# Optimization experiments

Hardware: AMD Instinct MI355X
Metric: run time of the kernel (lower is better)

The kernel has to match this reference:

```python
import jax, jax.numpy as jnp
import numpy as np

N, E = 50000, 800000
F_NODE, F_EDGE, H, LAT, MAXN = 128, 16, 128, 64, 200


def setup_inputs() -> dict:
    key = jax.random.key(0)
    ks = jax.random.split(key, 40)
    s = 0.05
    p = {
        'x': jax.random.normal(ks[0], (N, F_NODE), jnp.float32),
        'edge_index': jax.random.randint(ks[1], (2, E), 0, N, jnp.int64),
        'edge_attr': jax.random.normal(ks[2], (E, F_EDGE), jnp.float32),
        'eps': jax.random.normal(ks[3], (1, LAT), jnp.float32),
        'num_nodes': N,
        # GATConv layer 1 (heads=1)
        'W1': jax.random.normal(ks[4], (F_NODE, H), jnp.float32) * s,
        'att_src1': jax.random.normal(ks[5], (H,), jnp.float32) * s,
        'att_dst1': jax.random.normal(ks[6], (H,), jnp.float32) * s,
        'We1': jax.random.normal(ks[7], (F_EDGE, H), jnp.float32) * s,
        'att_e1': jax.random.normal(ks[8], (H,), jnp.float32) * s,
        'b1': jnp.zeros((H,), jnp.float32),
        # GATConv layer 2
        'W2': jax.random.normal(ks[9], (H, H), jnp.float32) * s,
        'att_src2': jax.random.normal(ks[10], (H,), jnp.float32) * s,
        'att_dst2': jax.random.normal(ks[11], (H,), jnp.float32) * s,
        'We2': jax.random.normal(ks[12], (F_EDGE, H), jnp.float32) * s,
        'att_e2': jax.random.normal(ks[13], (H,), jnp.float32) * s,
        'b2': jnp.zeros((H,), jnp.float32),
        # heads
        'mu_W': jax.random.normal(ks[14], (H, LAT), jnp.float32) * s,
        'mu_b': jnp.zeros((LAT,), jnp.float32),
        'lv_W': jax.random.normal(ks[15], (H, LAT), jnp.float32) * s,
        'lv_b': jnp.zeros((LAT,), jnp.float32),
        'dec_W': jax.random.normal(ks[16], (LAT, H), jnp.float32) * s,
        'dec_b': jnp.zeros((H,), jnp.float32),
        'adj_W1': jax.random.normal(ks[17], (H, H), jnp.float32) * s,
        'adj_b1': jnp.zeros((H,), jnp.float32),
        'adj_W2': jax.random.normal(ks[18], (H, MAXN), jnp.float32) * s,
        'adj_b2': jnp.zeros((MAXN,), jnp.float32),
        'nd_W1': jax.random.normal(ks[19], (H, H), jnp.float32) * s,
        'nd_b1': jnp.zeros((H,), jnp.float32),
        'nd_W2': jax.random.normal(ks[20], (H, F_NODE), jnp.float32) * s,
        'nd_b2': jnp.zeros((F_NODE,), jnp.float32),
    }
    return p


def _gat(h, src, dst, ea, W, a_s, a_d, We, a_e, b, n):
    # PyG GATConv, heads=1: linear transform, per-edge attention, segment softmax over dst
    g = h @ W                                     # [n, H]
    alpha = jax.nn.leaky_relu((g @ a_s)[src] + (g @ a_d)[dst] + (ea @ We) @ a_e,
                              negative_slope=0.2)  # [E']
    m = jax.ops.segment_max(alpha, dst, num_segments=n)
    ex = jnp.exp(alpha - m[dst])
    den = jax.ops.segment_sum(ex, dst, num_segments=n)
    w = ex / den[dst]
    return jax.ops.segment_sum(w[:, None] * g[src], dst, num_segments=n) + b


def _forward(x, edge_index, edge_attr, eps, num_nodes,
             W1, att_src1, att_dst1, We1, att_e1, b1,
             W2, att_src2, att_dst2, We2, att_e2, b2,
             mu_W, mu_b, lv_W, lv_b, dec_W, dec_b,
             adj_W1, adj_b1, adj_W2, adj_b2, nd_W1, nd_b1, nd_W2, nd_b2):
    n = x.shape[0]
    src, dst = edge_index[0], edge_index[1]
    # add self loops; self-loop edge_attr = per-node mean of incoming edge_attr (PyG fill_value='mean')
    deg = jax.ops.segment_sum(jnp.ones((src.shape[0],), x.dtype), dst, num_segments=n)
    mean_ea = jax.ops.segment_sum(edge_attr, dst, num_segments=n) / jnp.maximum(deg, 1.0)[:, None]
    loop = jnp.arange(n)
    src_f = jnp.concatenate([src, loop])
    dst_f = jnp.concatenate([dst, loop])
    ea_f = jnp.concatenate([edge_attr, mean_ea])
    h = jax.nn.relu(_gat(x, src_f, dst_f, ea_f, W1, att_src1, att_dst1, We1, att_e1, b1, n))
    h = jax.nn.relu(_gat(h, src_f, dst_f, ea_f, W2, att_src2, att_dst2, We2, att_e2, b2, n))
    hg = h.mean(axis=0, keepdims=True)            # global_mean_pool, single graph -> [1, H]
    mu = hg @ mu_W + mu_b
    logvar = hg @ lv_W + lv_b
    z = mu + eps * jnp.exp(0.5 * logvar)
    hd = jax.nn.relu(z @ dec_W + dec_b)           # [1, H]
    hn = jnp.broadcast_to(hd[:, None, :], (1, num_nodes, hd.shape[-1]))
    adj = jax.nn.relu(hn @ adj_W1 + adj_b1) @ adj_W2 + adj_b2   # [1, n, MAXN]
    adj = adj[:, :, :num_nodes]
    nodes = jax.nn.relu(hn @ nd_W1 + nd_b1) @ nd_W2 + nd_b2     # [1, n, F_NODE]
    return adj, nodes, mu, logvar


def reference(x, edge_index, edge_attr, eps, num_nodes,
              W1, att_src1, att_dst1, We1, att_e1, b1,
              W2, att_src2, att_dst2, We2, att_e2, b2,
              mu_W, mu_b, lv_W, lv_b, dec_W, dec_b,
              adj_W1, adj_b1, adj_W2, adj_b2, nd_W1, nd_b1, nd_W2, nd_b2):
    return _forward(x, edge_index, edge_attr, eps, num_nodes,
                    W1, att_src1, att_dst1, We1, att_e1, b1,
                    W2, att_src2, att_dst2, We2, att_e2, b2,
                    mu_W, mu_b, lv_W, lv_b, dec_W, dec_b,
                    adj_W1, adj_b1, adj_W2, adj_b2, nd_W1, nd_b1, nd_W2, nd_b2)
```

## Files before the change

kernel.cpp:

```cpp
#include <hip/hip_runtime.h>
#include <math.h>

#define NN   50000
#define EE   800000
#define EF   850000
#define HH   128
#define FE   16
#define LATD 64
#define MAXNN 200

#define ADJ_TOT   10000000
#define NODES_TOT 6400000
#define OUT_TOT   16400000
#define MU_OFF    16400000
#define LV_OFF    16400064

#define GEMMBLOCKS 782
#define DEGBLOCKS  782
#define NBSCAN     49

typedef __attribute__((ext_vector_type(8))) short bf16x8;
typedef __attribute__((ext_vector_type(4))) float f32x4;
typedef __attribute__((ext_vector_type(2))) float f32x2;

__device__ __forceinline__ unsigned short f2bf(float f){
  unsigned int u = __float_as_uint(f);
  unsigned int r = (u + 0x7FFFu + ((u>>16)&1u)) >> 16;
  return (unsigned short)r;
}
__device__ __forceinline__ float bf2f(unsigned short h){
  return __uint_as_float(((unsigned int)h)<<16);
}

__global__ __launch_bounds__(256) void kprep(int* ideg, float* hgsum,
                       const float* We1, const float* ae1, const float* We2, const float* ae2,
                       float* wa1, float* wa2,
                       const float* W1, const float* W2,
                       unsigned short* Wp1, unsigned short* Wp2){
  int i = blockIdx.x*256 + threadIdx.x;
  if(i < NN) ideg[i]=0;
  if(i < HH) hgsum[i]=0.f;
  if(i < FE){
    float s1=0.f, s2=0.f;
    for(int j=0;j<HH;j++){ s1 += We1[i*HH+j]*ae1[j]; s2 += We2[i*HH+j]*ae2[j]; }
    wa1[i]=s1; wa2[i]=s2;
  }
  if(i < HH*HH){
    int n = i >> 7, k = i & 127;
    Wp1[i] = f2bf(W1[k*HH + n]);
    Wp2[i] = f2bf(W2[k*HH + n]);
  }
}

__device__ __forceinline__ void gemm_body(int bid, int tid, const void* __restrict__ hin, int h_is_fp32,
    const unsigned short* __restrict__ Wp,
    const float* __restrict__ atts, const float* __restrict__ attd,
    unsigned char* __restrict__ A8, float* __restrict__ asrc, float* __restrict__ adst){
  int lane = tid & 63;
  int wid  = tid >> 6;
  int l = lane & 15, q = lane >> 4;
  int r0 = bid*64 + wid*16;
  if(r0 >= NN) return;
  const unsigned short* hb = (const unsigned short*)hin;
  const float*          hf = (const float*)hin;
  int row = r0 + l;

  bf16x8 afr[4];
  if(h_is_fp32){
    float4 u[8];
    #pragma unroll
    for(int kb=0;kb<4;kb++){
      const float* p = hf + (size_t)row*HH + kb*32 + q*8;
      u[kb*2]   = *(const float4*)(p);
      u[kb*2+1] = *(const float4*)(p+4);
    }
    #pragma unroll
    for(int kb=0;kb<4;kb++){
      afr[kb][0]=(short)f2bf(u[kb*2].x);   afr[kb][1]=(short)f2bf(u[kb*2].y);
      afr[kb][2]=(short)f2bf(u[kb*2].z);   afr[kb][3]=(short)f2bf(u[kb*2].w);
      afr[kb][4]=(short)f2bf(u[kb*2+1].x); afr[kb][5]=(short)f2bf(u[kb*2+1].y);
      afr[kb][6]=(short)f2bf(u[kb*2+1].z); afr[kb][7]=(short)f2bf(u[kb*2+1].w);
    }
  } else {
    #pragma unroll
    for(int kb=0;kb<4;kb++)
      afr[kb] = *(const bf16x8*)(hb + (size_t)row*HH + kb*32 + q*8);
  }

  f32x4 acc[8];
  #pragma unroll
  for(int t=0;t<8;t++) acc[t]=(f32x4){0.f,0.f,0.f,0.f};

  #pragma unroll
  for(int kb=0;kb<4;kb++){
    #pragma unroll
    for(int t=0;t<8;t++){
      bf16x8 b = *(const bf16x8*)(Wp + (size_t)(t*16+l)*HH + kb*32 + q*8);
      acc[t] = __builtin_amdgcn_mfma_f32_16x16x32_bf16(afr[kb], b, acc[t], 0,0,0);
    }
  }

  float av[8], dv[8];
  #pragma unroll
  for(int t=0;t<8;t++){ av[t]=atts[t*16+l]; dv[t]=attd[t*16+l]; }
  #pragma unroll
  for(int reg=0;reg<4;reg++){
    float ps=0.f, pd=0.f;
    #pragma unroll
    for(int t=0;t<8;t++){ ps+=acc[t][reg]*av[t]; pd+=acc[t][reg]*dv[t]; }
    #pragma unroll
    for(int m=8;m>=1;m>>=1){ ps+=__shfl_xor(ps,m,16); pd+=__shfl_xor(pd,m,16); }
    if(l==0){ int R=r0+q*4+reg; asrc[R]=ps; adst[R]=pd; }
  }
  #pragma unroll
  for(int t=0;t<8;t++)
    #pragma unroll
    for(int reg=0;reg<4;reg++){
      int pk = __builtin_amdgcn_cvt_pk_fp8_f32(acc[t][reg], 0.f, 0, false);
      A8[(size_t)(r0+q*4+reg)*HH + t*16 + l] = (unsigned char)(pk & 0xFF);
    }
}

__global__ __launch_bounds__(256) void kgemm3(const void* __restrict__ hin, int h_is_fp32,
    const unsigned short* __restrict__ Wp,
    const float* __restrict__ atts, const float* __restrict__ attd,
    unsigned char* __restrict__ A8, float* __restrict__ asrc, float* __restrict__ adst){
  gemm_body(blockIdx.x, threadIdx.x, hin, h_is_fp32, Wp, atts, attd, A8, asrc, adst);
}

__global__ __launch_bounds__(256) void kdeggemm(
    const int* __restrict__ ei, int* ideg, unsigned short* __restrict__ erank,
    const void* __restrict__ hin, int h_is_fp32,
    const unsigned short* __restrict__ Wp,
    const float* __restrict__ atts, const float* __restrict__ attd,
    unsigned char* __restrict__ A8, float* __restrict__ asrc, float* __restrict__ adst){
  if(blockIdx.x < GEMMBLOCKS){
    gemm_body(blockIdx.x, threadIdx.x, hin, h_is_fp32, Wp, atts, attd, A8, asrc, adst);
  } else {
    int e0 = ((blockIdx.x - GEMMBLOCKS)*256 + threadIdx.x)*4;
    if(e0 + 3 < EE){
      int4 d4 = *(const int4*)(ei + EE + e0);
      unsigned short r0 = (unsigned short)atomicAdd(&ideg[d4.x], 1);
      unsigned short r1 = (unsigned short)atomicAdd(&ideg[d4.y], 1);
      unsigned short r2 = (unsigned short)atomicAdd(&ideg[d4.z], 1);
      unsigned short r3 = (unsigned short)atomicAdd(&ideg[d4.w], 1);
      ushort4 rr; rr.x=r0; rr.y=r1; rr.z=r2; rr.w=r3;
      *(ushort4*)(erank + e0) = rr;
    } else {
      for(int j=0;j<4;j++)
        if(e0+j < EE) erank[e0+j] = (unsigned short)atomicAdd(&ideg[ei[EE+e0+j]], 1);
    }
  }
}

__global__ void kscan1(const int* __restrict__ ideg, int* rowstart, int* blocksum){
  __shared__ int sd[1024];
  int t=threadIdx.x; int i=blockIdx.x*1024+t;
  int v = (i<NN)? (ideg[i]+1) : 0;
  sd[t]=v; __syncthreads();
  for(int off=1; off<1024; off<<=1){
    int x = (t>=off)? sd[t-off] : 0;
    __syncthreads();
    sd[t] += x;
    __syncthreads();
  }
  if(i<NN) rowstart[i] = sd[t]-v;
  if(t==1023) blocksum[blockIdx.x]=sd[1023];
}
__global__ __launch_bounds__(256) void kscan3i(int* rowstart, const int* __restrict__ blocksum){
  __shared__ int bo[64];
  int t = threadIdx.x;
  if(t < 64){
    int v = (t < NBSCAN)? blocksum[t] : 0;
    int inc = v;
    #pragma unroll
    for(int off=1; off<64; off<<=1){
      int x = __shfl_up(inc, off);
      if(t>=off) inc += x;
    }
    bo[t] = inc - v;
  }
  __syncthreads();
  int i = blockIdx.x*256 + t;
  if(i<NN) rowstart[i] += bo[i>>10];
  if(i==0) rowstart[NN] = bo[NBSCAN];
}

__device__ __forceinline__ unsigned etpack(const float4* a4,
                         const float* __restrict__ wa1, const float* __restrict__ wa2){
  float4 v0=a4[0], v1=a4[1], v2=a4[2], v3=a4[3];
  float va[16]={v0.x,v0.y,v0.z,v0.w, v1.x,v1.y,v1.z,v1.w,
                v2.x,v2.y,v2.z,v2.w, v3.x,v3.y,v3.z,v3.w};
  float d1=0.f,d2=0.f;
  #pragma unroll
  for(int f=0;f<FE;f++){ d1+=va[f]*wa1[f]; d2+=va[f]*wa2[f]; }
  return (unsigned)f2bf(d1) | ((unsigned)f2bf(d2)<<16);
}
__global__ __launch_bounds__(256) void kscatter(const int* __restrict__ ei, const float* __restrict__ ea,
                         const float* __restrict__ wa1, const float* __restrict__ wa2,
                         const int* __restrict__ rowstart, const unsigned short* __restrict__ erank,
                         uint2* __restrict__ csr){
  int e0 = (blockIdx.x*256 + threadIdx.x)*2;
  if(e0>=EE) return;
  int sA=ei[e0],    sB=ei[e0+1];
  int dA=ei[EE+e0], dB=ei[EE+e0+1];
  int rA=(int)erank[e0], rB=(int)erank[e0+1];
  int pA=rowstart[dA]+rA, pB=rowstart[dB]+rB;
  const float4* a4 = (const float4*)(ea + (size_t)e0*FE);
  unsigned yA = etpack(a4,   wa1, wa2);
  unsigned yB = etpack(a4+4, wa1, wa2);
  uint2 enA; enA.x=(unsigned)sA; enA.y=yA;
  uint2 enB; enB.x=(unsigned)sB; enB.y=yB;
  csr[pA]=enA; csr[pB]=enB;
}

__global__ __launch_bounds__(256) void kgat(const unsigned char* __restrict__ A8,
    const float* __restrict__ asrc, const float* __restrict__ adst,
    const int* __restrict__ rowstart, uint2* __restrict__ csr,
    int mode, const float* __restrict__ bias,
    float* __restrict__ alphabuf, int* __restrict__ srcbuf,
    unsigned short* __restrict__ Bout){
  int lane = threadIdx.x & 63;
  int wid  = threadIdx.x >> 6;
  int i = blockIdx.x*4 + wid;
  if(i >= NN) return;
  int base = rowstart[i];
  int len  = rowstart[i+1]-base;
  float adi = adst[i];
  int lq = lane & 15;
  int qq = lane >> 4;
  float av[8];
  #pragma unroll
  for(int j=0;j<8;j++) av[j]=0.f;

  if(__builtin_expect(len <= 64, 1)){
    int P4 = (len+3)>>2;
    int nread = mode ? len : len-1;
    int s = i; float etlo = 0.f, ethi = 0.f;
    if(lane < nread){
      uint2 en = csr[base+lane];
      s = (int)en.x;
      etlo = bf2f((unsigned short)(en.y & 0xFFFFu));
      ethi = bf2f((unsigned short)(en.y >> 16));
    }
    float et = mode ? ethi : etlo;
    int skv0[6];
    #pragma unroll
    for(int j=0;j<6;j++) skv0[j] = (j<P4) ? __shfl(s, 4*j+qq) : i;
    unsigned ux[6], uy[6];
    #pragma unroll
    for(int j=0;j<6;j++){
      uint2 u = *(const uint2*)(A8 + (size_t)skv0[j]*HH + lq*8);
      ux[j]=u.x; uy[j]=u.y;
    }
    if(!mode){
      float e1 = (lane < len-1) ? etlo : 0.f;
      float e2 = (lane < len-1) ? ethi : 0.f;
      #pragma unroll
      for(int mk=32;mk>=1;mk>>=1){ e1 += __shfl_xor(e1,mk); e2 += __shfl_xor(e2,mk); }
      float dg = fmaxf((float)(len-1), 1.f);
      float m1 = e1/dg, m2 = e2/dg;
      if(lane == len-1){
        et = m1;
        uint2 se; se.x=(unsigned)i;
        se.y=(unsigned)f2bf(m1) | ((unsigned)f2bf(m2)<<16);
        csr[base+len-1] = se;
      }
    }
    float a = -1e30f;
    if(lane < len){
      a = asrc[s] + adi + et;
      a = fmaxf(a, 0.2f*a);
    }
    float m = a;
    #pragma unroll
    for(int mk=32;mk>=1;mk>>=1) m = fmaxf(m, __shfl_xor(m,mk));
    float ex = (lane<len) ? __expf(a-m) : 0.f;
    float sm = ex;
    #pragma unroll
    for(int mk=32;mk>=1;mk>>=1) sm += __shfl_xor(sm,mk);
    ex *= __builtin_amdgcn_rcpf(sm);

    float w0[6];
    #pragma unroll
    for(int j=0;j<6;j++) w0[j] = (j<P4) ? __shfl(ex, 4*j+qq) : 0.f;
    #pragma unroll
    for(int j=0;j<6;j++){
      f32x2 v;
      v=__builtin_amdgcn_cvt_pk_f32_fp8((int)ux[j],false); av[0]+=w0[j]*v[0]; av[1]+=w0[j]*v[1];
      v=__builtin_amdgcn_cvt_pk_f32_fp8((int)ux[j],true ); av[2]+=w0[j]*v[0]; av[3]+=w0[j]*v[1];
      v=__builtin_amdgcn_cvt_pk_f32_fp8((int)uy[j],false); av[4]+=w0[j]*v[0]; av[5]+=w0[j]*v[1];
      v=__builtin_amdgcn_cvt_pk_f32_fp8((int)uy[j],true ); av[6]+=w0[j]*v[0]; av[7]+=w0[j]*v[1];
    }
    for(int t0=6; t0<P4; t0+=6){
      int skv[6]; float w[6];
      #pragma unroll
      for(int j=0;j<6;j++){
        if(t0+j < P4){
          int idx = 4*(t0+j) + qq;
          skv[j] = __shfl(s, idx);
          w[j]   = __shfl(ex, idx);
        } else { skv[j] = i; w[j] = 0.f; }
      }
      unsigned vx[6], vy[6];
      #pragma unroll
      for(int j=0;j<6;j++){
        uint2 u = *(const uint2*)(A8 + (size_t)skv[j]*HH + lq*8);
        vx[j]=u.x; vy[j]=u.y;
      }
      #pragma unroll
      for(int j=0;j<6;j++){
        f32x2 v;
        v=__builtin_amdgcn_cvt_pk_f32_fp8((int)vx[j],false); av[0]+=w[j]*v[0]; av[1]+=w[j]*v[1];
        v=__builtin_amdgcn_cvt_pk_f32_fp8((int)vx[j],true ); av[2]+=w[j]*v[0]; av[3]+=w[j]*v[1];
        v=__builtin_amdgcn_cvt_pk_f32_fp8((int)vy[j],false); av[4]+=w[j]*v[0]; av[5]+=w[j]*v[1];
        v=__builtin_amdgcn_cvt_pk_f32_fp8((int)vy[j],true ); av[6]+=w[j]*v[0]; av[7]+=w[j]*v[1];
      }
    }
  } else {
    int deg = len-1;
    int lim = mode ? len : deg;
    float lm = -1e30f, e1 = 0.f, e2 = 0.f;
    for(int k=lane;k<lim;k+=64){
      uint2 en = csr[base+k];
      int sr = (int)en.x;
      float lo = bf2f((unsigned short)(en.y & 0xFFFFu));
      float hi = bf2f((unsigned short)(en.y >> 16));
      float etv = mode ? hi : lo;
      if(!mode){ e1 += lo; e2 += hi; }
      float a = asrc[sr] + adi + etv;
      a = fmaxf(a, 0.2f*a);
      alphabuf[base+k]=a; srcbuf[base+k]=sr;
      lm = fmaxf(lm,a);
    }
    #pragma unroll
    for(int mk=32;mk>=1;mk>>=1){
      e1 += __shfl_xor(e1,mk);
      e2 += __shfl_xor(e2,mk);
      lm  = fmaxf(lm, __shfl_xor(lm,mk));
    }
    float aself = 0.f;
    if(!mode){
      float m1 = e1/(float)deg, m2 = e2/(float)deg;
      aself = asrc[i] + adi + m1;
      aself = fmaxf(aself, 0.2f*aself);
      lm = fmaxf(lm, aself);
      if(lane==0){
        uint2 se; se.x=(unsigned)i;
        se.y=(unsigned)f2bf(m1) | ((unsigned)f2bf(m2)<<16);
        csr[base+deg] = se;
      }
    }
    float ls=0.f;
    for(int k=lane;k<len;k+=64){
      float a;
      if(mode) a = alphabuf[base+k];
      else     a = (k<deg)? alphabuf[base+k] : aself;
      float e_ = __expf(a-lm);
      alphabuf[base+k]=e_;
      ls += e_;
    }
    #pragma unroll
    for(int mk=32;mk>=1;mk>>=1) ls += __shfl_xor(ls,mk);
    float inv = 1.f/ls;
    int lim2 = mode ? len : deg;
    int P4 = (len+3)>>2;
    for(int t=0;t<P4;t++){
      int k = 4*t + qq;
      int sk = i; float wk = 0.f;
      if(k<len){
        sk = (k<lim2)? srcbuf[base+k] : i;
        wk = alphabuf[base+k]*inv;
      }
      uint2 u = *(const uint2*)(A8 + (size_t)sk*HH + lq*8);
      f32x2 v;
      v=__builtin_amdgcn_cvt_pk_f32_fp8((int)u.x,false); av[0]+=wk*v[0]; av[1]+=wk*v[1];
      v=__builtin_amdgcn_cvt_pk_f32_fp8((int)u.x,true ); av[2]+=wk*v[0]; av[3]+=wk*v[1];
      v=__builtin_amdgcn_cvt_pk_f32_fp8((int)u.y,false); av[4]+=wk*v[0]; av[5]+=wk*v[1];
      v=__builtin_amdgcn_cvt_pk_f32_fp8((int)u.y,true ); av[6]+=wk*v[0]; av[7]+=wk*v[1];
    }
  }

  #pragma unroll
  for(int j=0;j<8;j++){
    av[j] += __shfl_xor(av[j],16);
    av[j] += __shfl_xor(av[j],32);
  }
  if(qq==0){
    const float4* bp = (const float4*)(bias + lq*8);
    float4 b0=bp[0], b1=bp[1];
    float o0=fmaxf(av[0]+b0.x,0.f), o1=fmaxf(av[1]+b0.y,0.f);
    float o2=fmaxf(av[2]+b0.z,0.f), o3=fmaxf(av[3]+b0.w,0.f);
    float o4=fmaxf(av[4]+b1.x,0.f), o5=fmaxf(av[5]+b1.y,0.f);
    float o6=fmaxf(av[6]+b1.z,0.f), o7=fmaxf(av[7]+b1.w,0.f);
    uint4 ov;
    ov.x=(unsigned)f2bf(o0)|((unsigned)f2bf(o1)<<16);
    ov.y=(unsigned)f2bf(o2)|((unsigned)f2bf(o3)<<16);
    ov.z=(unsigned)f2bf(o4)|((unsigned)f2bf(o5)<<16);
    ov.w=(unsigned)f2bf(o6)|((unsigned)f2bf(o7)<<16);
    *(uint4*)(Bout + (size_t)i*HH + lq*8) = ov;
  }
}

__global__ __launch_bounds__(256) void khg(const unsigned short* __restrict__ B, float* hgsum){
  int f = threadIdx.x & 127;
  int half = threadIdx.x >> 7;
  float s=0.f;
  for(int i = blockIdx.x*2+half; i < NN; i += gridDim.x*2)
    s += bf2f(B[(size_t)i*HH + f]);
  __shared__ float sd[256];
  sd[threadIdx.x]=s; __syncthreads();
  if(half==0) atomicAdd(&hgsum[f], sd[threadIdx.x]+sd[threadIdx.x+128]);
}

__global__ __launch_bounds__(256) void kdec(const float* __restrict__ hgsum, const float* __restrict__ eps,
   const float* muW,const float* mub,const float* lvW,const float* lvb,
   const float* decW,const float* decb,
   const float* aW1,const float* ab1,const float* aW2,const float* ab2,
   const float* nW1,const float* nb1,const float* nW2,const float* nb2,
   float* out, float* rowadj, float* rownodes){
  __shared__ float hg[HH], z[LATD], hd[HH], t1[HH], t2[HH];
  int t=threadIdx.x;
  if(t<HH) hg[t]=hgsum[t]*(1.0f/NN);
  __syncthreads();
  if(t<LATD){
    float mu=mub[t], lv=lvb[t];
    #pragma unroll 8
    for(int k=0;k<HH;k++){ mu += hg[k]*muW[k*LATD+t]; lv += hg[k]*lvW[k*LATD+t]; }
    out[MU_OFF+t]=mu; out[LV_OFF+t]=lv;
    z[t]=mu + eps[t]*expf(0.5f*lv);
  }
  __syncthreads();
  if(t<HH){
    float a=decb[t];
    #pragma unroll 8
    for(int k=0;k<LATD;k++) a += z[k]*decW[k*HH+t];
    hd[t]=fmaxf(a,0.f);
  }
  __syncthreads();
  if(t<HH){
    float a=ab1[t];
    #pragma unroll 8
    for(int k=0;k<HH;k++) a += hd[k]*aW1[k*HH+t];
    t1[t]=fmaxf(a,0.f);
  } else {
    int j=t-HH;
    float a=nb1[j];
    #pragma unroll 8
    for(int k=0;k<HH;k++) a += hd[k]*nW1[k*HH+j];
    t2[j]=fmaxf(a,0.f);
  }
  __syncthreads();
  for(int j=t;j<MAXNN;j+=256){
    float a=ab2[j];
    #pragma unroll 8
    for(int k=0;k<HH;k++) a += t1[k]*aW2[k*MAXNN+j];
    rowadj[j]=a;
  }
  if(t<HH){
    float a=nb2[t];
    #pragma unroll 8
    for(int k=0;k<HH;k++) a += t2[k]*nW2[k*HH+t];
    rownodes[t]=a;
  }
}

__global__ __launch_bounds__(256) void kbcast(const float* __restrict__ rowadj,
                                              const float* __restrict__ rownodes,
                                              float* __restrict__ out){
  __shared__ float row[MAXNN+HH];
  int t=threadIdx.x;
  if(t<MAXNN) row[t]=rowadj[t];
  if(t<HH) row[MAXNN+t]=rownodes[t];
  __syncthreads();
  int stride=gridDim.x*blockDim.x;
  const int tot4 = OUT_TOT/4;
  for(int q=blockIdx.x*blockDim.x+t; q<tot4; q+=stride){
    int idx = q*4;
    float4 vv;
    if(idx<ADJ_TOT){
      int j = idx % MAXNN;
      vv = *(const float4*)&row[j];
    } else {
      int j = (idx-ADJ_TOT) & (HH-1);
      vv = *(const float4*)&row[MAXNN+j];
    }
    *(float4*)&out[idx] = vv;
  }
}

extern "C" void kernel_launch(void* const* d_in, const int* in_sizes, int n_in,
                              void* d_out, int out_size, void* d_ws, size_t ws_size,
                              hipStream_t stream){
  const float* x   = (const float*)d_in[0];
  const int*   ei  = (const int*)d_in[1];
  const float* ea  = (const float*)d_in[2];
  const float* eps = (const float*)d_in[3];
  const float* W1  =(const float*)d_in[5];
  const float* as1 =(const float*)d_in[6];
  const float* ad1 =(const float*)d_in[7];
  const float* We1 =(const float*)d_in[8];
  const float* ae1 =(const float*)d_in[9];
  const float* b1  =(const float*)d_in[10];
  const float* W2  =(const float*)d_in[11];
  const float* as2 =(const float*)d_in[12];
  const float* ad2 =(const float*)d_in[13];
  const float* We2 =(const float*)d_in[14];
  const float* ae2 =(const float*)d_in[15];
  const float* b2  =(const float*)d_in[16];
  const float* muW =(const float*)d_in[17];
  const float* mub =(const float*)d_in[18];
  const float* lvW =(const float*)d_in[19];
  const float* lvb =(const float*)d_in[20];
  const float* decW=(const float*)d_in[21];
  const float* decb=(const float*)d_in[22];
  const float* aW1 =(const float*)d_in[23];
  const float* ab1 =(const float*)d_in[24];
  const float* aW2 =(const float*)d_in[25];
  const float* ab2 =(const float*)d_in[26];
  const float* nW1 =(const float*)d_in[27];
  const float* nb1 =(const float*)d_in[28];
  const float* nW2 =(const float*)d_in[29];
  const float* nb2 =(const float*)d_in[30];
  float* out=(float*)d_out;

  char* w=(char*)d_ws;
  unsigned char*  A8  = (unsigned char*)w;  w += (size_t)NN*HH;
  unsigned short* Bbf = (unsigned short*)w; w += (size_t)NN*HH*2;
  unsigned short* Wp1 = (unsigned short*)w; w += (size_t)HH*HH*2;
  unsigned short* Wp2 = (unsigned short*)w; w += (size_t)HH*HH*2;
  uint2*  csr      = (uint2*)w;  w += (size_t)EF*8;
  float*  alphabuf = (float*)w;  w += (size_t)EF*4;
  int*    srcbuf   = (int*)w;    w += (size_t)EF*4;
  unsigned short* erank = (unsigned short*)w; w += (size_t)EE*2;
  int*    rowstart = (int*)w;    w += (size_t)(NN+1)*4;
  int*    ideg     = (int*)w;    w += (size_t)NN*4;
  float*  hgsum    = (float*)w;  w += 128*4;
  float*  asrc     = (float*)w;  w += (size_t)NN*4;
  float*  adst     = (float*)w;  w += (size_t)NN*4;
  float*  wa1      = (float*)w;  w += 16*4;
  float*  wa2      = (float*)w;  w += 16*4;
  float*  rowadj   = (float*)w;  w += 256*4;
  float*  rownodes = (float*)w;  w += 128*4;
  int*    blocksum = (int*)w;    w += 64*4;

  int gatblocks  = (NN+3)/4;

  hipLaunchKernelGGL(kprep, dim3((NN+255)/256), dim3(256), 0, stream,
                     ideg, hgsum, We1, ae1, We2, ae2, wa1, wa2, W1, W2, Wp1, Wp2);
  hipLaunchKernelGGL(kdeggemm, dim3(GEMMBLOCKS+DEGBLOCKS), dim3(256), 0, stream,
                     ei, ideg, erank,
                     (const void*)x, 1, Wp1, as1, ad1, A8, asrc, adst);
  hipLaunchKernelGGL(kscan1, dim3(NBSCAN), dim3(1024), 0, stream, ideg, rowstart, blocksum);
  hipLaunchKernelGGL(kscan3i, dim3((NN+255)/256), dim3(256), 0, stream, rowstart, blocksum);
  hipLaunchKernelGGL(kscatter, dim3((EE/2+255)/256), dim3(256), 0, stream,
                     ei, ea, wa1, wa2, rowstart, erank, csr);
  hipLaunchKernelGGL(kgat,  dim3(gatblocks), dim3(256), 0, stream,
                     A8, asrc, adst, rowstart, csr, 0, b1, alphabuf, srcbuf, Bbf);
  hipLaunchKernelGGL(kgemm3, dim3(GEMMBLOCKS), dim3(256), 0, stream,
                     (const void*)Bbf, 0, Wp2, as2, ad2, A8, asrc, adst);
  hipLaunchKernelGGL(kgat,  dim3(gatblocks), dim3(256), 0, stream,
                     A8, asrc, adst, rowstart, csr, 1, b2, alphabuf, srcbuf, Bbf);
  hipLaunchKernelGGL(khg,   dim3(512), dim3(256), 0, stream, Bbf, hgsum);
  hipLaunchKernelGGL(kdec,  dim3(1), dim3(256), 0, stream, hgsum, eps,
                     muW,mub,lvW,lvb,decW,decb,aW1,ab1,aW2,ab2,nW1,nb1,nW2,nb2,
                     out, rowadj, rownodes);
  hipLaunchKernelGGL(kbcast, dim3(2048), dim3(256), 0, stream, rowadj, rownodes, out);
}
```

Measured before the change: 414.3 us.

## Process two GAT destination nodes per wavefront using 32-lane halves

The GAT aggregation kernel now assigns each destination node to half a wavefront (32 lanes) instead of a full 64-lane wavefront. Each block therefore covers 8 nodes, and the grid shrinks to match. Shuffle reductions are narrowed to width 32, and each lane group gathers two source rows per step instead of four. With typical degrees around 17, the aim is to stop leaving most lanes idle. The trade-off is possible divergence when the two halves take different degree paths, and more serial gather iterations per node.

```diff
diff --git a/kernel.cpp b/kernel.cpp
--- a/kernel.cpp
+++ b/kernel.cpp
@@ -222,23 +222,25 @@
     unsigned short* __restrict__ Bout){
   int lane = threadIdx.x & 63;
   int wid  = threadIdx.x >> 6;
-  int i = blockIdx.x*4 + wid;
+  int half = lane >> 5;
+  int hl   = lane & 31;
+  int i = blockIdx.x*8 + wid*2 + half;
   if(i >= NN) return;
   int base = rowstart[i];
   int len  = rowstart[i+1]-base;
   float adi = adst[i];
-  int lq = lane & 15;
-  int qq = lane >> 4;
+  int lq = hl & 15;
+  int qq = hl >> 4;
   float av[8];
   #pragma unroll
   for(int j=0;j<8;j++) av[j]=0.f;
 
-  if(__builtin_expect(len <= 64, 1)){
-    int P4 = (len+3)>>2;
+  if(__builtin_expect(len <= 32, 1)){
+    int P2 = (len+1)>>1;
     int nread = mode ? len : len-1;
     int s = i; float etlo = 0.f, ethi = 0.f;
-    if(lane < nread){
-      uint2 en = csr[base+lane];
+    if(hl < nread){
+      uint2 en = csr[base+hl];
       s = (int)en.x;
       etlo = bf2f((unsigned short)(en.y & 0xFFFFu));
       ethi = bf2f((unsigned short)(en.y >> 16));
@@ -246,7 +248,7 @@
     float et = mode ? ethi : etlo;
     int skv0[6];
     #pragma unroll
-    for(int j=0;j<6;j++) skv0[j] = (j<P4) ? __shfl(s, 4*j+qq) : i;
+    for(int j=0;j<6;j++) skv0[j] = (j<P2) ? __shfl(s, 2*j+qq, 32) : i;
     unsigned ux[6], uy[6];
     #pragma unroll
     for(int j=0;j<6;j++){
@@ -254,13 +256,13 @@
       ux[j]=u.x; uy[j]=u.y;
     }
     if(!mode){
-      float e1 = (lane < len-1) ? etlo : 0.f;
-      float e2 = (lane < len-1) ? ethi : 0.f;
+      float e1 = (hl < len-1) ? etlo : 0.f;
+      float e2 = (hl < len-1) ? ethi : 0.f;
       #pragma unroll
-      for(int mk=32;mk>=1;mk>>=1){ e1 += __shfl_xor(e1,mk); e2 += __shfl_xor(e2,mk); }
+      for(int mk=16;mk>=1;mk>>=1){ e1 += __shfl_xor(e1,mk); e2 += __shfl_xor(e2,mk); }
       float dg = fmaxf((float)(len-1), 1.f);
       float m1 = e1/dg, m2 = e2/dg;
-      if(lane == len-1){
+      if(hl == len-1){
         et = m1;
         uint2 se; se.x=(unsigned)i;
         se.y=(unsigned)f2bf(m1) | ((unsigned)f2bf(m2)<<16);
@@ -268,22 +270,22 @@
       }
     }
     float a = -1e30f;
-    if(lane < len){
+    if(hl < len){
       a = asrc[s] + adi + et;
       a = fmaxf(a, 0.2f*a);
     }
     float m = a;
     #pragma unroll
-    for(int mk=32;mk>=1;mk>>=1) m = fmaxf(m, __shfl_xor(m,mk));
-    float ex = (lane<len) ? __expf(a-m) : 0.f;
+    for(int mk=16;mk>=1;mk>>=1) m = fmaxf(m, __shfl_xor(m,mk));
+    float ex = (hl<len) ? __expf(a-m) : 0.f;
     float sm = ex;
     #pragma unroll
-    for(int mk=32;mk>=1;mk>>=1) sm += __shfl_xor(sm,mk);
+    for(int mk=16;mk>=1;mk>>=1) sm += __shfl_xor(sm,mk);
     ex *= __builtin_amdgcn_rcpf(sm);
 
     float w0[6];
     #pragma unroll
-    for(int j=0;j<6;j++) w0[j] = (j<P4) ? __shfl(ex, 4*j+qq) : 0.f;
+    for(int j=0;j<6;j++) w0[j] = (j<P2) ? __shfl(ex, 2*j+qq, 32) : 0.f;
     #pragma unroll
     for(int j=0;j<6;j++){
       f32x2 v;
@@ -292,14 +294,14 @@
       v=__builtin_amdgcn_cvt_pk_f32_fp8((int)uy[j],false); av[4]+=w0[j]*v[0]; av[5]+=w0[j]*v[1];
       v=__builtin_amdgcn_cvt_pk_f32_fp8((int)uy[j],true ); av[6]+=w0[j]*v[0]; av[7]+=w0[j]*v[1];
     }
-    for(int t0=6; t0<P4; t0+=6){
+    for(int t0=6; t0<P2; t0+=6){
       int skv[6]; float w[6];
       #pragma unroll
       for(int j=0;j<6;j++){
-        if(t0+j < P4){
-          int idx = 4*(t0+j) + qq;
-          skv[j] = __shfl(s, idx);
-          w[j]   = __shfl(ex, idx);
+        if(t0+j < P2){
+          int idx = 2*(t0+j) + qq;
+          skv[j] = __shfl(s, idx, 32);
+          w[j]   = __shfl(ex, idx, 32);
         } else { skv[j] = i; w[j] = 0.f; }
       }
       unsigned vx[6], vy[6];
@@ -321,7 +323,7 @@
     int deg = len-1;
     int lim = mode ? len : deg;
     float lm = -1e30f, e1 = 0.f, e2 = 0.f;
-    for(int k=lane;k<lim;k+=64){
+    for(int k=hl;k<lim;k+=32){
       uint2 en = csr[base+k];
       int sr = (int)en.x;
       float lo = bf2f((unsigned short)(en.y & 0xFFFFu));
@@ -334,7 +336,7 @@
       lm = fmaxf(lm,a);
     }
     #pragma unroll
-    for(int mk=32;mk>=1;mk>>=1){
+    for(int mk=16;mk>=1;mk>>=1){
       e1 += __shfl_xor(e1,mk);
       e2 += __shfl_xor(e2,mk);
       lm  = fmaxf(lm, __shfl_xor(lm,mk));
@@ -345,14 +347,14 @@
       aself = asrc[i] + adi + m1;
       aself = fmaxf(aself, 0.2f*aself);
       lm = fmaxf(lm, aself);
-      if(lane==0){
+      if(hl==0){
         uint2 se; se.x=(unsigned)i;
         se.y=(unsigned)f2bf(m1) | ((unsigned)f2bf(m2)<<16);
         csr[base+deg] = se;
       }
     }
     float ls=0.f;
-    for(int k=lane;k<len;k+=64){
+    for(int k=hl;k<len;k+=32){
       float a;
       if(mode) a = alphabuf[base+k];
       else     a = (k<deg)? alphabuf[base+k] : aself;
@@ -361,12 +363,12 @@
       ls += e_;
     }
     #pragma unroll
-    for(int mk=32;mk>=1;mk>>=1) ls += __shfl_xor(ls,mk);
+    for(int mk=16;mk>=1;mk>>=1) ls += __shfl_xor(ls,mk);
     float inv = 1.f/ls;
     int lim2 = mode ? len : deg;
-    int P4 = (len+3)>>2;
-    for(int t=0;t<P4;t++){
-      int k = 4*t + qq;
+    int P2 = (len+1)>>1;
+    for(int t=0;t<P2;t++){
+      int k = 2*t + qq;
       int sk = i; float wk = 0.f;
       if(k<len){
         sk = (k<lim2)? srcbuf[base+k] : i;
@@ -382,10 +384,7 @@
   }
 
   #pragma unroll
-  for(int j=0;j<8;j++){
-    av[j] += __shfl_xor(av[j],16);
-    av[j] += __shfl_xor(av[j],32);
-  }
+  for(int j=0;j<8;j++) av[j] += __shfl_xor(av[j],16);
   if(qq==0){
     const float4* bp = (const float4*)(bias + lq*8);
     float4 b0=bp[0], b1=bp[1];
@@ -544,7 +543,7 @@
   float*  rownodes = (float*)w;  w += 128*4;
   int*    blocksum = (int*)w;    w += 64*4;
 
-  int gatblocks  = (NN+3)/4;
+  int gatblocks  = (NN+7)/8;
 
   hipLaunchKernelGGL(kprep, dim3((NN+255)/256), dim3(256), 0, stream,
                      ideg, hgsum, We1, ae1, We2, ae2, wa1, wa2, W1, W2, Wp1, Wp2);
```

After: 403.3 us. -2.6%, faster.
